# Performance work log

Measured on AMD Instinct MI355X. Metric: run time of the kernel, lower is better.

Reference implementation:

```python
import jax, jax.numpy as jnp
import numpy as np

OBJ_DIM = 1024
NUM_REL_CLS = 8
N_OBJ = 4096
N_PAIRS = 65536


def setup_inputs() -> dict:
    key = jax.random.key(0)
    k1, k2, k3, k4, k5, k6 = jax.random.split(key, 6)
    obj_feats = jax.random.normal(k1, (N_OBJ, OBJ_DIM), dtype=jnp.float32)
    pairs = jax.random.randint(k2, (N_PAIRS, 2), 0, N_OBJ, dtype=jnp.int64)
    # proto_support_detector params: Linear(2*obj_dim -> obj_dim), Linear(obj_dim -> num_rel_cls)
    s1 = 1.0 / np.sqrt(2 * OBJ_DIM)
    s2 = 1.0 / np.sqrt(OBJ_DIM)
    W1 = jax.random.uniform(k3, (OBJ_DIM, 2 * OBJ_DIM), jnp.float32, -s1, s1)
    b1 = jax.random.uniform(k4, (OBJ_DIM,), jnp.float32, -s1, s1)
    W2 = jax.random.uniform(k5, (NUM_REL_CLS, OBJ_DIM), jnp.float32, -s2, s2)
    b2 = jax.random.uniform(k6, (NUM_REL_CLS,), jnp.float32, -s2, s2)
    return {"obj_feats": obj_feats, "pairs": pairs, "W1": W1, "b1": b1, "W2": W2, "b2": b2}


def reference(obj_feats, pairs, W1, b1, W2, b2):
    # Batched form of the per-pair proto_support_detector calls:
    #   rel_feat = Linear(cat([sub, obj], -1)); rel_dist = Linear(rel_feat)
    sub = obj_feats[pairs[:, 0]]                      # [P, D] gather
    obj = obj_feats[pairs[:, 1]]                      # [P, D] gather
    rel_feat = jnp.concatenate([sub, obj], axis=-1)   # [P, 2D]
    rel_feat = rel_feat @ W1.T + b1                   # [P, D]
    rel_dist = rel_feat @ W2.T + b2                   # [P, C]
    return rel_dist
```

## Files before the change

### kernel.cpp

```cpp
#include <hip/hip_runtime.h>

#define OBJ_DIM 1024
#define NREL 8
#define NOBJ 4096
#define NPAIRS 65536

#define WC_OFF   0
#define CVEC_OFF 16384
#define PROJ_OFF 16400


__global__ __launch_bounds__(256) void prep_kernel(
    const float* __restrict__ W1, const float* __restrict__ W2,
    const float* __restrict__ b1, float* __restrict__ Wc,
    float* __restrict__ cvec)
{
    const int cblk = blockIdx.x & 7;
    const int kblk = blockIdx.x >> 3;
    const int c  = cblk * 256 + threadIdx.x;
    const int k0 = kblk * 32;

    float acc[NREL];
#pragma unroll
    for (int r = 0; r < NREL; ++r) acc[r] = 0.f;

#pragma unroll 8
    for (int kk = 0; kk < 32; ++kk) {
        const int k = k0 + kk;
        const float w1 = W1[(size_t)k * 2048 + c];
#pragma unroll
        for (int r = 0; r < NREL; ++r)
            acc[r] += W2[r * 1024 + k] * w1;
    }
#pragma unroll
    for (int r = 0; r < NREL; ++r)
        atomicAdd(&Wc[r * 2048 + c], acc[r]);

    if (cblk == 0 && threadIdx.x < 32) {
        const int k = k0 + (int)threadIdx.x;
        const float bb = b1[k];
#pragma unroll
        for (int r = 0; r < NREL; ++r) {
            float v = W2[r * 1024 + k] * bb;
            v += __shfl_down(v, 16);
            v += __shfl_down(v, 8);
            v += __shfl_down(v, 4);
            v += __shfl_down(v, 2);
            v += __shfl_down(v, 1);
            if (threadIdx.x == 0) atomicAdd(&cvec[r], v);
        }
    }
}

__global__ __launch_bounds__(256) void proj_kernel(
    const float* __restrict__ obj, const float* __restrict__ Wc,
    float* __restrict__ proj)
{
    __shared__ float sh[16 * 1024];

    const int t = threadIdx.x;
#pragma unroll
    for (int i = 0; i < 16; ++i) {
        const int f4 = t + 256 * i;
        const int f  = f4 * 4;
        const int r   = f >> 11;
        const int rem = f & 2047;
        const int h   = rem >> 10;
        const int k   = rem & 1023;
        const float4 v = ((const float4*)Wc)[f4];
        *((float4*)&sh[(h * 8 + r) * 1024 + k]) = v;
    }
    __syncthreads();

    const int wave = t >> 6, lane = t & 63;
    const int n0 = blockIdx.x * 8 + wave * 2;
    const float4* xa = (const float4*)(obj + (size_t)n0 * 1024);
    const float4* xb = xa + 256;

    float4 x0[4], x1[4];
#pragma unroll
    for (int i = 0; i < 4; ++i) {
        x0[i] = xa[lane + 64 * i];
        x1[i] = xb[lane + 64 * i];
    }

    float a0[16], a1[16];
#pragma unroll
    for (int q = 0; q < 16; ++q) {
        float s0 = 0.f, s1 = 0.f;
        const float4* wq = (const float4*)(sh + q * 1024);
#pragma unroll
        for (int i = 0; i < 4; ++i) {
            const float4 w = wq[lane + 64 * i];
            s0 += w.x * x0[i].x + w.y * x0[i].y + w.z * x0[i].z + w.w * x0[i].w;
            s1 += w.x * x1[i].x + w.y * x1[i].y + w.z * x1[i].z + w.w * x1[i].w;
        }
        a0[q] = s0;
        a1[q] = s1;
    }
    __syncthreads();

    float* scr = sh + wave * 2304;
#pragma unroll
    for (int q4 = 0; q4 < 16; q4 += 4) {
        float4 w0 = make_float4(a0[q4], a0[q4 + 1], a0[q4 + 2], a0[q4 + 3]);
        float4 w1 = make_float4(a1[q4], a1[q4 + 1], a1[q4 + 2], a1[q4 + 3]);
        *((float4*)&scr[lane * 36 + q4])      = w0;
        *((float4*)&scr[lane * 36 + 16 + q4]) = w1;
    }
    __syncthreads();

    const int o = lane >> 1, half = lane & 1;
    float s = 0.f;
#pragma unroll 8
    for (int j = 0; j < 32; ++j)
        s += scr[(half * 32 + j) * 36 + o];
    s += __shfl_down(s, 1);
    if (half == 0) {
        const int row = o >> 4, q = o & 15;
        proj[(size_t)(n0 + row) * 16 + q] = s;
    }
}

__global__ __launch_bounds__(256) void gather_kernel(
    const int* __restrict__ pairs, const float* __restrict__ proj,
    const float* __restrict__ cvec, const float* __restrict__ b2,
    float* __restrict__ out)
{
    const int p = blockIdx.x * 256 + threadIdx.x;

    const int2 ij = ((const int2*)pairs)[p];

    const float4 c0 = ((const float4*)cvec)[0];
    const float4 c1 = ((const float4*)cvec)[1];
    const float4 d0 = ((const float4*)b2)[0];
    const float4 d1 = ((const float4*)b2)[1];

    const float4* ps = (const float4*)(proj + (size_t)ij.x * 16);
    const float4* po = (const float4*)(proj + (size_t)ij.y * 16 + 8);
    const float4 s0 = ps[0], s1 = ps[1];
    const float4 o0 = po[0], o1 = po[1];

    float4 r0, r1;
    r0.x = s0.x + o0.x + c0.x + d0.x;
    r0.y = s0.y + o0.y + c0.y + d0.y;
    r0.z = s0.z + o0.z + c0.z + d0.z;
    r0.w = s0.w + o0.w + c0.w + d0.w;
    r1.x = s1.x + o1.x + c1.x + d1.x;
    r1.y = s1.y + o1.y + c1.y + d1.y;
    r1.z = s1.z + o1.z + c1.z + d1.z;
    r1.w = s1.w + o1.w + c1.w + d1.w;

    ((float4*)out)[(size_t)p * 2]     = r0;
    ((float4*)out)[(size_t)p * 2 + 1] = r1;
}

extern "C" void kernel_launch(void* const* d_in, const int* in_sizes, int n_in,
                              void* d_out, int out_size, void* d_ws, size_t ws_size,
                              hipStream_t stream) {
    const float* obj   = (const float*)d_in[0];
    const int*   pairs = (const int*)d_in[1];
    const float* W1    = (const float*)d_in[2];
    const float* b1    = (const float*)d_in[3];
    const float* W2    = (const float*)d_in[4];
    const float* b2    = (const float*)d_in[5];
    float* out = (float*)d_out;

    float* ws   = (float*)d_ws;
    float* Wc   = ws + WC_OFF;
    float* cvec = ws + CVEC_OFF;
    float* proj = ws + PROJ_OFF;

    hipMemsetAsync(ws, 0, (size_t)(CVEC_OFF + 16) * sizeof(float), stream);

    prep_kernel<<<256, 256, 0, stream>>>(W1, W2, b1, Wc, cvec);
    proj_kernel<<<512, 256, 0, stream>>>(obj, Wc, proj);
    gather_kernel<<<NPAIRS / 256, 256, 0, stream>>>(pairs, proj, cvec, b2, out);
}
```

Baseline: 96.49 us.

## Drop atomics and memset, fold biases into proj, compute four rows per wave

The prep kernel now reduces the W2·W1 partial products in shared memory and writes Wc directly in the layout proj uses, instead of using global atomicAdd on a zeroed buffer. That removes the memset and the atomic traffic. Wc can then be staged into LDS with direct global-to-LDS loads. The proj kernel processes four object rows per wave, reusing each LDS weight read across more rows, and adds the combined bias (W2·b1 + b2) so the gather kernel only sums two projections. The costs are higher register pressure and only half as many proj blocks, which leaves less latency hiding per CU.

```diff
diff --git a/kernel.cpp b/kernel.cpp
--- a/kernel.cpp
+++ b/kernel.cpp
@@ -6,135 +6,179 @@
 #define NPAIRS 65536
 
 #define WC_OFF   0
-#define CVEC_OFF 16384
+#define CADD_OFF 16384
 #define PROJ_OFF 16400
 
+
+__device__ __forceinline__ void stage16(const void* g, void* l) {
+    __builtin_amdgcn_global_load_lds(
+        (const __attribute__((address_space(1))) void*)g,
+        (__attribute__((address_space(3))) void*)l,
+        16, 0, 0);
+}
 
 __global__ __launch_bounds__(256) void prep_kernel(
     const float* __restrict__ W1, const float* __restrict__ W2,
-    const float* __restrict__ b1, float* __restrict__ Wc,
-    float* __restrict__ cvec)
+    const float* __restrict__ b1, const float* __restrict__ b2,
+    float* __restrict__ Wc, float* __restrict__ cadd)
 {
-    const int cblk = blockIdx.x & 7;
-    const int kblk = blockIdx.x >> 3;
-    const int c  = cblk * 256 + threadIdx.x;
-    const int k0 = kblk * 32;
-
-    float acc[NREL];
-#pragma unroll
-    for (int r = 0; r < NREL; ++r) acc[r] = 0.f;
-
+    __shared__ float part[256 * 33];
+
+    const int t = threadIdx.x;
+    const int b = blockIdx.x;
+
+    if (b < 256) {
+        const int cq = t & 1;
+        const int kg = t >> 1;
+        const float4* W14 = (const float4*)W1;
+
+        float w2r[8][8];
+#pragma unroll
+        for (int r = 0; r < 8; ++r) {
+            const float4* w2p = (const float4*)(W2 + r * 1024 + kg * 8);
+            const float4 wa = w2p[0], wb = w2p[1];
+            w2r[r][0] = wa.x; w2r[r][1] = wa.y; w2r[r][2] = wa.z; w2r[r][3] = wa.w;
+            w2r[r][4] = wb.x; w2r[r][5] = wb.y; w2r[r][6] = wb.z; w2r[r][7] = wb.w;
+        }
+
+        float acc[8][4] = {};
+#pragma unroll
+        for (int kk = 0; kk < 8; ++kk) {
+            const int k = kg * 8 + kk;
+            const float4 w1 = W14[(size_t)k * 512 + b * 2 + cq];
+#pragma unroll
+            for (int r = 0; r < 8; ++r) {
+                acc[r][0] += w2r[r][kk] * w1.x;
+                acc[r][1] += w2r[r][kk] * w1.y;
+                acc[r][2] += w2r[r][kk] * w1.z;
+                acc[r][3] += w2r[r][kk] * w1.w;
+            }
+        }
+
+#pragma unroll
+        for (int r = 0; r < 8; ++r)
+#pragma unroll
+            for (int c = 0; c < 4; ++c)
+                part[t * 33 + r * 4 + c] = acc[r][c];
+        __syncthreads();
+
+        if (t < 64) {
+            const int r = t >> 3, cc = t & 7;
+            const int cqo = cc >> 2, j = (r << 2) + (cc & 3);
+            float s0 = 0.f, s1 = 0.f;
 #pragma unroll 8
-    for (int kk = 0; kk < 32; ++kk) {
-        const int k = k0 + kk;
-        const float w1 = W1[(size_t)k * 2048 + c];
-#pragma unroll
-        for (int r = 0; r < NREL; ++r)
-            acc[r] += W2[r * 1024 + k] * w1;
-    }
-#pragma unroll
-    for (int r = 0; r < NREL; ++r)
-        atomicAdd(&Wc[r * 2048 + c], acc[r]);
-
-    if (cblk == 0 && threadIdx.x < 32) {
-        const int k = k0 + (int)threadIdx.x;
-        const float bb = b1[k];
-#pragma unroll
-        for (int r = 0; r < NREL; ++r) {
-            float v = W2[r * 1024 + k] * bb;
-            v += __shfl_down(v, 16);
-            v += __shfl_down(v, 8);
-            v += __shfl_down(v, 4);
-            v += __shfl_down(v, 2);
-            v += __shfl_down(v, 1);
-            if (threadIdx.x == 0) atomicAdd(&cvec[r], v);
+            for (int u = 0; u < 128; u += 2) {
+                s0 += part[((u    ) * 2 + cqo) * 33 + j];
+                s1 += part[((u + 1) * 2 + cqo) * 33 + j];
+            }
+            const int cglob = b * 8 + cc;
+            const int h = cglob >> 10, kcol = cglob & 1023;
+            Wc[(h * 8 + r) * 1024 + kcol] = s0 + s1;
+        }
+    } else {
+        const float4 bv = ((const float4*)b1)[t];
+        float acc[8];
+#pragma unroll
+        for (int r = 0; r < 8; ++r) {
+            const float4 w = ((const float4*)(W2 + r * 1024))[t];
+            acc[r] = w.x * bv.x + w.y * bv.y + w.z * bv.z + w.w * bv.w;
+        }
+#pragma unroll
+        for (int r = 0; r < 8; ++r) part[t * 9 + r] = acc[r];
+        __syncthreads();
+        if (t < 64) {
+            const int r = t & 7, g = t >> 3;
+            float s = 0.f;
+#pragma unroll 8
+            for (int u = 0; u < 32; ++u) s += part[(g * 32 + u) * 9 + r];
+            s += __shfl_down(s, 32);
+            s += __shfl_down(s, 16);
+            s += __shfl_down(s, 8);
+            if (g == 0) cadd[r] = s + b2[r];
         }
     }
 }
 
 __global__ __launch_bounds__(256) void proj_kernel(
     const float* __restrict__ obj, const float* __restrict__ Wc,
-    float* __restrict__ proj)
+    const float* __restrict__ cadd, float* __restrict__ proj)
 {
     __shared__ float sh[16 * 1024];
 
     const int t = threadIdx.x;
-#pragma unroll
-    for (int i = 0; i < 16; ++i) {
-        const int f4 = t + 256 * i;
-        const int f  = f4 * 4;
-        const int r   = f >> 11;
-        const int rem = f & 2047;
-        const int h   = rem >> 10;
-        const int k   = rem & 1023;
-        const float4 v = ((const float4*)Wc)[f4];
-        *((float4*)&sh[(h * 8 + r) * 1024 + k]) = v;
+    const float4* Wc4 = (const float4*)Wc;
+    float4* sh4 = (float4*)sh;
+#pragma unroll
+    for (int i = 0; i < 16; ++i)
+        stage16(&Wc4[t + 256 * i], &sh4[t + 256 * i]);
+    __syncthreads();
+
+    const int wave = t >> 6, lane = t & 63;
+    const int n0 = blockIdx.x * 16 + wave * 4;
+    const float4* xrow = (const float4*)(obj + (size_t)n0 * 1024);
+
+    float4 x[4][4];
+#pragma unroll
+    for (int r = 0; r < 4; ++r)
+#pragma unroll
+        for (int i = 0; i < 4; ++i)
+            x[r][i] = xrow[r * 256 + lane + 64 * i];
+
+    float a[4][16];
+#pragma unroll
+    for (int r = 0; r < 4; ++r)
+#pragma unroll
+        for (int q = 0; q < 16; ++q) a[r][q] = 0.f;
+
+#pragma unroll
+    for (int q = 0; q < 16; ++q) {
+        const float4* wq = (const float4*)(sh + q * 1024);
+#pragma unroll
+        for (int i = 0; i < 4; ++i) {
+            const float4 w = wq[lane + 64 * i];
+#pragma unroll
+            for (int r = 0; r < 4; ++r)
+                a[r][q] += w.x * x[r][i].x + w.y * x[r][i].y
+                         + w.z * x[r][i].z + w.w * x[r][i].w;
+        }
     }
     __syncthreads();
 
-    const int wave = t >> 6, lane = t & 63;
-    const int n0 = blockIdx.x * 8 + wave * 2;
-    const float4* xa = (const float4*)(obj + (size_t)n0 * 1024);
-    const float4* xb = xa + 256;
-
-    float4 x0[4], x1[4];
-#pragma unroll
-    for (int i = 0; i < 4; ++i) {
-        x0[i] = xa[lane + 64 * i];
-        x1[i] = xb[lane + 64 * i];
-    }
-
-    float a0[16], a1[16];
-#pragma unroll
-    for (int q = 0; q < 16; ++q) {
-        float s0 = 0.f, s1 = 0.f;
-        const float4* wq = (const float4*)(sh + q * 1024);
-#pragma unroll
-        for (int i = 0; i < 4; ++i) {
-            const float4 w = wq[lane + 64 * i];
-            s0 += w.x * x0[i].x + w.y * x0[i].y + w.z * x0[i].z + w.w * x0[i].w;
-            s1 += w.x * x1[i].x + w.y * x1[i].y + w.z * x1[i].z + w.w * x1[i].w;
-        }
-        a0[q] = s0;
-        a1[q] = s1;
-    }
-    __syncthreads();
-
     float* scr = sh + wave * 2304;
 #pragma unroll
-    for (int q4 = 0; q4 < 16; q4 += 4) {
-        float4 w0 = make_float4(a0[q4], a0[q4 + 1], a0[q4 + 2], a0[q4 + 3]);
-        float4 w1 = make_float4(a1[q4], a1[q4 + 1], a1[q4 + 2], a1[q4 + 3]);
-        *((float4*)&scr[lane * 36 + q4])      = w0;
-        *((float4*)&scr[lane * 36 + 16 + q4]) = w1;
-    }
-    __syncthreads();
-
-    const int o = lane >> 1, half = lane & 1;
-    float s = 0.f;
+    for (int pass = 0; pass < 2; ++pass) {
+        const int ra = pass * 2, rb = pass * 2 + 1;
+#pragma unroll
+        for (int q4 = 0; q4 < 16; q4 += 4) {
+            *((float4*)&scr[lane * 36 + q4]) =
+                make_float4(a[ra][q4], a[ra][q4 + 1], a[ra][q4 + 2], a[ra][q4 + 3]);
+            *((float4*)&scr[lane * 36 + 16 + q4]) =
+                make_float4(a[rb][q4], a[rb][q4 + 1], a[rb][q4 + 2], a[rb][q4 + 3]);
+        }
+        __syncthreads();
+
+        const int o = lane >> 1, half = lane & 1;
+        float s = 0.f;
 #pragma unroll 8
-    for (int j = 0; j < 32; ++j)
-        s += scr[(half * 32 + j) * 36 + o];
-    s += __shfl_down(s, 1);
-    if (half == 0) {
-        const int row = o >> 4, q = o & 15;
-        proj[(size_t)(n0 + row) * 16 + q] = s;
+        for (int j = 0; j < 32; ++j)
+            s += scr[(half * 32 + j) * 36 + o];
+        s += __shfl_down(s, 1);
+        if (half == 0) {
+            const int row = o >> 4, q = o & 15;
+            const float v = s + (q < 8 ? cadd[q] : 0.f);
+            proj[(size_t)(n0 + ra + row) * 16 + q] = v;
+        }
+        __syncthreads();
     }
 }
 
 __global__ __launch_bounds__(256) void gather_kernel(
     const int* __restrict__ pairs, const float* __restrict__ proj,
-    const float* __restrict__ cvec, const float* __restrict__ b2,
     float* __restrict__ out)
 {
     const int p = blockIdx.x * 256 + threadIdx.x;
 
     const int2 ij = ((const int2*)pairs)[p];
-
-    const float4 c0 = ((const float4*)cvec)[0];
-    const float4 c1 = ((const float4*)cvec)[1];
-    const float4 d0 = ((const float4*)b2)[0];
-    const float4 d1 = ((const float4*)b2)[1];
 
     const float4* ps = (const float4*)(proj + (size_t)ij.x * 16);
     const float4* po = (const float4*)(proj + (size_t)ij.y * 16 + 8);
@@ -142,14 +186,10 @@
     const float4 o0 = po[0], o1 = po[1];
 
     float4 r0, r1;
-    r0.x = s0.x + o0.x + c0.x + d0.x;
-    r0.y = s0.y + o0.y + c0.y + d0.y;
-    r0.z = s0.z + o0.z + c0.z + d0.z;
-    r0.w = s0.w + o0.w + c0.w + d0.w;
-    r1.x = s1.x + o1.x + c1.x + d1.x;
-    r1.y = s1.y + o1.y + c1.y + d1.y;
-    r1.z = s1.z + o1.z + c1.z + d1.z;
-    r1.w = s1.w + o1.w + c1.w + d1.w;
+    r0.x = s0.x + o0.x;  r0.y = s0.y + o0.y;
+    r0.z = s0.z + o0.z;  r0.w = s0.w + o0.w;
+    r1.x = s1.x + o1.x;  r1.y = s1.y + o1.y;
+    r1.z = s1.z + o1.z;  r1.w = s1.w + o1.w;
 
     ((float4*)out)[(size_t)p * 2]     = r0;
     ((float4*)out)[(size_t)p * 2 + 1] = r1;
@@ -168,12 +208,11 @@
 
     float* ws   = (float*)d_ws;
     float* Wc   = ws + WC_OFF;
-    float* cvec = ws + CVEC_OFF;
+    float* cadd = ws + CADD_OFF;
     float* proj = ws + PROJ_OFF;
 
-    hipMemsetAsync(ws, 0, (size_t)(CVEC_OFF + 16) * sizeof(float), stream);
-
-    prep_kernel<<<256, 256, 0, stream>>>(W1, W2, b1, Wc, cvec);
-    proj_kernel<<<512, 256, 0, stream>>>(obj, Wc, proj);
-    gather_kernel<<<NPAIRS / 256, 256, 0, stream>>>(pairs, proj, cvec, b2, out);
-}
+
+    prep_kernel<<<257, 256, 0, stream>>>(W1, W2, b1, b2, Wc, cadd);
+    proj_kernel<<<256, 256, 0, stream>>>(obj, Wc, cadd, proj);
+    gather_kernel<<<NPAIRS / 256, 256, 0, stream>>>(pairs, proj, out);
+}
```

New measurement: 89.49 us. -7.3%, faster.
